# Performance work log

Measured on AMD Instinct MI355X. Metric: run time of the kernel, lower is better.

The kernel has to match this reference:

```python
import jax, jax.numpy as jnp
import numpy as np

N_NODES = 100000
N_EDGES = 1600000
IN_CH = 128
HIDDEN = 64
N_CLASSES = 40


def setup_inputs() -> dict:
    key = jax.random.key(0)
    k_x, k_e, k_w1, k_w2 = jax.random.split(key, 4)
    x = jax.random.normal(k_x, (N_NODES, IN_CH), dtype=jnp.float32)
    edge_index = jax.random.randint(k_e, (2, N_EDGES), 0, N_NODES, dtype=jnp.int64)
    # Glorot-style init for GCN weights
    W1 = jax.random.normal(k_w1, (IN_CH, HIDDEN), dtype=jnp.float32) * (1.0 / np.sqrt(IN_CH))
    b1 = jnp.zeros((HIDDEN,), dtype=jnp.float32)
    W2 = jax.random.normal(k_w2, (HIDDEN, N_CLASSES), dtype=jnp.float32) * (1.0 / np.sqrt(HIDDEN))
    b2 = jnp.zeros((N_CLASSES,), dtype=jnp.float32)
    return {"x": x, "edge_index": edge_index, "W1": W1, "b1": b1, "W2": W2, "b2": b2}


def reference(x, edge_index, W1, b1, W2, b2):
    n = x.shape[0]
    # PyG GCNConv: add self-loops, symmetric degree normalization
    loop = jnp.arange(n, dtype=edge_index.dtype)
    src = jnp.concatenate([edge_index[0], loop])  # message sources j
    dst = jnp.concatenate([edge_index[1], loop])  # aggregation targets i
    w = jnp.ones(src.shape[0], dtype=x.dtype)     # edge_weight=None -> ones
    deg = jax.ops.segment_sum(w, dst, num_segments=n)
    dinv = jnp.where(deg > 0, jax.lax.rsqrt(jnp.maximum(deg, 1e-12)), 0.0)
    norm = dinv[src] * dinv[dst]                  # [E+N]

    def gcn_conv(h, W, b):
        hw = h @ W                                # transform first (fewer flops)
        msg = hw[src] * norm[:, None]             # gather + normalize
        return jax.ops.segment_sum(msg, dst, num_segments=n) + b  # scatter-add

    h = jax.nn.relu(gcn_conv(x, W1, b1))
    # dropout is identity in eval mode
    out = gcn_conv(h, W2, b2)
    return out
```

## Files before the change

### kernel.cpp

```cpp
#include <hip/hip_runtime.h>
#include <hip/hip_bf16.h>

#define NNODES 100000
#define NEDGES 1600000
#define IN_CH 128
#define HID 64
#define NC 40
#define NPAD 100352
#define NBUK 196
#define CAP 9216
#define BCHUNK 4096
#define NBIN 391

typedef unsigned short ushort_t;
typedef unsigned int uint_t;
typedef __attribute__((ext_vector_type(8))) short short8;
typedef __attribute__((ext_vector_type(4))) float floatx4;
typedef __attribute__((ext_vector_type(2))) float f32x2;

__device__ __forceinline__ ushort_t f2bf(float f) {
    union { float ff; unsigned int i; } t;
    t.ff = f;
    unsigned int r = t.i + 0x7fff + ((t.i >> 16) & 1);
    return (ushort_t)(r >> 16);
}
__device__ __forceinline__ void acc2(f32x2& a, uint_t p) {
    union { unsigned int i; float f; } lo, hi;
    lo.i = p << 16;
    hi.i = p & 0xffff0000u;
    f32x2 v = {lo.f, hi.f};
    a += v;
}

__global__ __launch_bounds__(256) void k_bin0(
    const int* __restrict__ srcs, const int* __restrict__ dsts,
    int* __restrict__ gcur, uint_t* __restrict__ tmp, int e,
    const float* __restrict__ W1, ushort_t* __restrict__ Wp,
    ushort_t* __restrict__ hb, int n)
{
    __shared__ uint_t pk[BCHUNK];
    __shared__ ushort_t bk[BCHUNK];
    __shared__ int hist[NBUK];
    __shared__ int base[NBUK];
    int t = threadIdx.x;
    if (blockIdx.x >= NBIN) {
        for (int i = t; i < IN_CH * HID; i += 256) {
            int j = i & 7;
            int m = (i >> 3) & 15;
            int ct = (i >> 7) & 3;
            int quad = (i >> 9) & 3;
            int kc = i >> 11;
            int k = kc * 32 + quad * 8 + j;
            int c = ct * 16 + m;
            Wp[i] = f2bf(W1[k * HID + c]);
        }
        uint_t* hbz = (uint_t*)(hb + (size_t)n * HID);
        if (t < 32) hbz[t] = 0;
        return;
    }
    int begin = blockIdx.x * BCHUNK;
    int cnt = e - begin; if (cnt > BCHUNK) cnt = BCHUNK;

    for (int i = t; i < NBUK; i += 256) hist[i] = 0;
    __syncthreads();
    for (int j = t; j < cnt; j += 256) {
        int d = dsts[begin + j];
        int s = srcs[begin + j];
        int b = d >> 9;
        pk[j] = (uint_t)s | ((uint_t)(d & 511) << 17);
        bk[j] = (ushort_t)b;
        atomicAdd(&hist[b], 1);
    }
    __syncthreads();
    for (int i = t; i < NBUK; i += 256) {
        base[i] = i * CAP + atomicAdd(&gcur[i], hist[i]);
        hist[i] = 0;
    }
    __syncthreads();
    for (int j = t; j < cnt; j += 256) {
        int b = bk[j];
        int r = atomicAdd(&hist[b], 1);
        int pos = base[b] + r;
        if (pos < (b + 1) * CAP) tmp[pos] = pk[j];
    }
}

__global__ __launch_bounds__(256) void k_sort(
    const uint_t* __restrict__ tmp, const int* __restrict__ gcur,
    int* __restrict__ row_start, float* __restrict__ dinv,
    uint_t* __restrict__ es, int n, int e)
{
    __shared__ int cnt[512];
    __shared__ int sc[512];
    __shared__ int red[256];
    int t = threadIdx.x;
    int b = blockIdx.x;
    int d0 = b << 9;
    int total = gcur[b];
    if (total > CAP) total = CAP;
    int part = 0;
    for (int i = t; i < b; i += 256) part += gcur[i];
    red[t] = part;
    cnt[t] = 0; cnt[t + 256] = 0;
    __syncthreads();
    for (int off = 128; off > 0; off >>= 1) {
        if (t < off) red[t] += red[t + off];
        __syncthreads();
    }
    int gb = red[0];
    const uint_t* seg = tmp + b * CAP;
    for (int j = t; j < total; j += 256)
        atomicAdd(&cnt[seg[j] >> 17], 1);
    __syncthreads();
    sc[t] = cnt[t]; sc[t + 256] = cnt[t + 256];
    __syncthreads();
    for (int off = 1; off < 512; off <<= 1) {
        int v0 = (t >= off) ? sc[t - off] : 0;
        int i1 = t + 256;
        int v1 = (i1 >= off) ? sc[i1 - off] : 0;
        __syncthreads();
        sc[t] += v0; sc[i1] += v1;
        __syncthreads();
    }
#pragma unroll
    for (int q = 0; q < 2; ++q) {
        int i = t + q * 256;
        int node = d0 + i;
        int start = gb + sc[i] - cnt[i];
        if (node < n) {
            row_start[node] = start;
            dinv[node] = rsqrtf((float)cnt[i] + 1.0f);
        }
        cnt[i] = start;
    }
    __syncthreads();
    for (int j = t; j < total; j += 256) {
        uint_t p = seg[j];
        int ld = (int)(p >> 17);
        int pos = atomicAdd(&cnt[ld], 1);
        es[pos] = p & 0x1FFFFu;
    }
    if (b == NBUK - 1 && t == 0) row_start[n] = e;
}

__global__ __launch_bounds__(256) void k_gemm1(
    const float* __restrict__ x, const ushort_t* __restrict__ Wp,
    const float* __restrict__ dinv, ushort_t* __restrict__ hw1, int n)
{
    int wave = threadIdx.x >> 6;
    int lane = threadIdx.x & 63;
    int m = lane & 15;
    int quad = lane >> 4;
    int row = blockIdx.x * 64 + wave * 16 + m;
    int rowc = row < n ? row : (n - 1);
    const float* xr = x + (size_t)rowc * IN_CH + quad * 8;

    floatx4 acc[4];
#pragma unroll
    for (int ct = 0; ct < 4; ++ct) acc[ct] = (floatx4){0.f, 0.f, 0.f, 0.f};

#pragma unroll
    for (int kc = 0; kc < 4; ++kc) {
        float4 xa = *(const float4*)(xr + kc * 32);
        float4 xb = *(const float4*)(xr + kc * 32 + 4);
        short8 a;
        a[0] = (short)f2bf(xa.x); a[1] = (short)f2bf(xa.y);
        a[2] = (short)f2bf(xa.z); a[3] = (short)f2bf(xa.w);
        a[4] = (short)f2bf(xb.x); a[5] = (short)f2bf(xb.y);
        a[6] = (short)f2bf(xb.z); a[7] = (short)f2bf(xb.w);
#pragma unroll
        for (int ct = 0; ct < 4; ++ct) {
            short8 b = *(const short8*)(Wp + ((((kc * 4 + quad) * 4 + ct) * 16 + m) << 3));
            acc[ct] = __builtin_amdgcn_mfma_f32_16x16x32_bf16(a, b, acc[ct], 0, 0, 0);
        }
    }
    int r0 = blockIdx.x * 64 + wave * 16 + quad * 4;
#pragma unroll
    for (int r = 0; r < 4; ++r) {
        int rr = r0 + r;
        if (rr < n) {
            float di = dinv[rr];
            ushort_t* o = hw1 + (size_t)rr * HID + m;
#pragma unroll
            for (int ct = 0; ct < 4; ++ct) o[ct * 16] = f2bf(acc[ct][r] * di);
        } else if (rr == n) {
            ushort_t* o = hw1 + (size_t)n * HID + m;
#pragma unroll
            for (int ct = 0; ct < 4; ++ct) o[ct * 16] = 0;
        }
    }
}

__global__ __launch_bounds__(256) void k_agg1(
    const int* __restrict__ row_start, const uint_t* __restrict__ es,
    const float* __restrict__ dinv, const uint_t* __restrict__ hw1u,
    const float* __restrict__ b1, ushort_t* __restrict__ hb, int n)
{
    int lane = threadIdx.x & 63;
    int obase = lane & 56;
    int ol = lane & 7;
    int node = blockIdx.x * 32 + (threadIdx.x >> 3);
    bool valid = node < n;
    int rs = valid ? row_start[node] : 0;
    int re = valid ? row_start[node + 1] : 0;
    float di = valid ? dinv[node] : 0.f;
    int selfrow = valid ? node : n;

    f32x2 c0, c1, c2, c3;
    {
        uint4 sp = *(const uint4*)(hw1u + (size_t)selfrow * 32 + ol * 4);
        c0 = (f32x2){0.f, 0.f}; c1 = c0; c2 = c0; c3 = c0;
        acc2(c0, sp.x); acc2(c1, sp.y); acc2(c2, sp.z); acc2(c3, sp.w);
    }
    for (int base = rs; base < re; base += 8) {
        int idx = base + ol;
        int el = (idx < re) ? (int)es[idx] : n;
        uint4 p[8];
#pragma unroll
        for (int b = 0; b < 8; ++b) {
            int s = __shfl(el, obase + b);
            p[b] = *(const uint4*)(hw1u + (size_t)s * 32 + ol * 4);
        }
#pragma unroll
        for (int b = 0; b < 8; ++b) {
            acc2(c0, p[b].x); acc2(c1, p[b].y);
            acc2(c2, p[b].z); acc2(c3, p[b].w);
        }
    }
    if (valid) {
        float4 bb0 = ((const float4*)b1)[ol * 2];
        float4 bb1 = ((const float4*)b1)[ol * 2 + 1];
        float h0 = fmaxf(c0.x * di + bb0.x, 0.f);
        float h1 = fmaxf(c0.y * di + bb0.y, 0.f);
        float h2 = fmaxf(c1.x * di + bb0.z, 0.f);
        float h3 = fmaxf(c1.y * di + bb0.w, 0.f);
        float h4 = fmaxf(c2.x * di + bb1.x, 0.f);
        float h5 = fmaxf(c2.y * di + bb1.y, 0.f);
        float h6 = fmaxf(c3.x * di + bb1.z, 0.f);
        float h7 = fmaxf(c3.y * di + bb1.w, 0.f);
        uint4 st;
        st.x = (uint_t)f2bf(h0 * di) | ((uint_t)f2bf(h1 * di) << 16);
        st.y = (uint_t)f2bf(h2 * di) | ((uint_t)f2bf(h3 * di) << 16);
        st.z = (uint_t)f2bf(h4 * di) | ((uint_t)f2bf(h5 * di) << 16);
        st.w = (uint_t)f2bf(h6 * di) | ((uint_t)f2bf(h7 * di) << 16);
        *(uint4*)(hb + (size_t)node * HID + ol * 8) = st;
    }
}

__global__ __launch_bounds__(256) void k_agg2(
    const int* __restrict__ row_start, const uint_t* __restrict__ es,
    const float* __restrict__ dinv, const uint_t* __restrict__ hbu,
    const float* __restrict__ W2, const float* __restrict__ b2,
    float* __restrict__ out, int n)
{
    __shared__ float wsm[HID * NC];
    __shared__ float hsm[32][68];
    for (int i = threadIdx.x; i < HID * NC; i += 256) wsm[i] = W2[i];
    __syncthreads();

    int lane = threadIdx.x & 63;
    int obase = lane & 56;
    int ol = lane & 7;
    int slot = threadIdx.x >> 3;
    int node = blockIdx.x * 32 + slot;
    bool valid = node < n;
    int rs = valid ? row_start[node] : 0;
    int re = valid ? row_start[node + 1] : 0;
    float di = valid ? dinv[node] : 0.f;
    int selfrow = valid ? node : n;

    f32x2 c0, c1, c2, c3;
    {
        uint4 sp = *(const uint4*)(hbu + (size_t)selfrow * 32 + ol * 4);
        c0 = (f32x2){0.f, 0.f}; c1 = c0; c2 = c0; c3 = c0;
        acc2(c0, sp.x); acc2(c1, sp.y); acc2(c2, sp.z); acc2(c3, sp.w);
    }
    for (int base = rs; base < re; base += 8) {
        int idx = base + ol;
        int el = (idx < re) ? (int)es[idx] : n;
        uint4 p[8];
#pragma unroll
        for (int b = 0; b < 8; ++b) {
            int s = __shfl(el, obase + b);
            p[b] = *(const uint4*)(hbu + (size_t)s * 32 + ol * 4);
        }
#pragma unroll
        for (int b = 0; b < 8; ++b) {
            acc2(c0, p[b].x); acc2(c1, p[b].y);
            acc2(c2, p[b].z); acc2(c3, p[b].w);
        }
    }
    {
        float4 g0, g1;
        g0.x = c0.x * di; g0.y = c0.y * di; g0.z = c1.x * di; g0.w = c1.y * di;
        g1.x = c2.x * di; g1.y = c2.y * di; g1.z = c3.x * di; g1.w = c3.y * di;
        *(float4*)&hsm[slot][ol * 8] = g0;
        *(float4*)&hsm[slot][ol * 8 + 4] = g1;
    }
    int w8 = (threadIdx.x >> 6) * 8;
    int qm = lane >> 4;
    int lq = lane & 15;
    int lw = (lq < 10) ? lq : 0;
    const float4* w4 = (const float4*)wsm;
#pragma unroll
    for (int pass = 0; pass < 2; ++pass) {
        int slot2 = w8 + pass * 4 + qm;
        int node2 = blockIdx.x * 32 + slot2;
        float4 acc = ((const float4*)b2)[lw];
#pragma unroll 4
        for (int k4 = 0; k4 < 16; ++k4) {
            float4 hk = *(const float4*)&hsm[slot2][k4 * 4];
            float4 w0 = w4[(k4 * 4 + 0) * 10 + lw];
            float4 w1 = w4[(k4 * 4 + 1) * 10 + lw];
            float4 w2 = w4[(k4 * 4 + 2) * 10 + lw];
            float4 w3 = w4[(k4 * 4 + 3) * 10 + lw];
            acc.x += hk.x * w0.x + hk.y * w1.x + hk.z * w2.x + hk.w * w3.x;
            acc.y += hk.x * w0.y + hk.y * w1.y + hk.z * w2.y + hk.w * w3.y;
            acc.z += hk.x * w0.z + hk.y * w1.z + hk.z * w2.z + hk.w * w3.z;
            acc.w += hk.x * w0.w + hk.y * w1.w + hk.z * w2.w + hk.w * w3.w;
        }
        if (node2 < n && lq < 10)
            *(float4*)(out + (size_t)node2 * NC + lq * 4) = acc;
    }
}

extern "C" void kernel_launch(void* const* d_in, const int* in_sizes, int n_in,
                              void* d_out, int out_size, void* d_ws, size_t ws_size,
                              hipStream_t stream) {
    const float* x  = (const float*)d_in[0];
    const int* edge = (const int*)d_in[1];
    const float* W1 = (const float*)d_in[2];
    const float* b1 = (const float*)d_in[3];
    const float* W2 = (const float*)d_in[4];
    const float* b2 = (const float*)d_in[5];
    float* out      = (float*)d_out;

    const int n = in_sizes[0] / IN_CH;
    const int e = in_sizes[1] / 2;
    const int* srcs = edge;
    const int* dsts = edge + e;

    int*      gcur      = (int*)d_ws;
    int*      row_start = gcur + 256;
    float*    dinv      = (float*)(row_start + NPAD);
    uint_t*   tmp       = (uint_t*)(dinv + NPAD);
    uint_t*   es        = tmp + (size_t)NBUK * CAP;
    ushort_t* Wp        = (ushort_t*)(es + NEDGES);
    ushort_t* hw1       = Wp + 8192;
    ushort_t* hb        = hw1 + (size_t)(NNODES + 1) * HID;

    hipMemsetAsync(gcur, 0, NBUK * sizeof(int), stream);
    k_bin0<<<NBIN + 1, 256, 0, stream>>>(srcs, dsts, gcur, tmp, e, W1, Wp, hb, n);
    k_sort<<<NBUK, 256, 0, stream>>>(tmp, gcur, row_start, dinv, es, n, e);
    k_gemm1<<<(n + 63) / 64, 256, 0, stream>>>(x, Wp, dinv, hw1, n);
    k_agg1<<<(n + 31) / 32, 256, 0, stream>>>(row_start, es, dinv, (const uint_t*)hw1, b1, hb, n);
    k_agg2<<<(n + 31) / 32, 256, 0, stream>>>(row_start, es, dinv, (const uint_t*)hb, W2, b2, out, n);
}
```

Before: 220.8 us.

## Sort nodes by degree within block and double-buffer neighbor gathers in aggregation

Both aggregation kernels now rank the block's 32 nodes by in-degree and give them to 8-lane groups in that order, so nodes with similar degrees share a wavefront and there is less loop divergence. The gather loop becomes a two-stage software pipeline: indices are loaded as vectors and the next 8 rows are fetched while the previous 8 are accumulated. Launch bounds request 2 blocks per CU. The cost is an in-block rank sort with two extra barriers and higher register pressure from the doubled gather buffers. The tail handling now clamps out-of-range nodes to n-1, which recomputes and rewrites that node instead of using the padding row.

```diff
diff --git a/kernel.cpp b/kernel.cpp
--- a/kernel.cpp
+++ b/kernel.cpp
@@ -17,6 +17,7 @@
 typedef __attribute__((ext_vector_type(8))) short short8;
 typedef __attribute__((ext_vector_type(4))) float floatx4;
 typedef __attribute__((ext_vector_type(2))) float f32x2;
+typedef unsigned int uint4u __attribute__((ext_vector_type(4))) __attribute__((aligned(4)));
 
 __device__ __forceinline__ ushort_t f2bf(float f) {
     union { float ff; unsigned int i; } t;
@@ -30,6 +31,30 @@
     hi.i = p & 0xffff0000u;
     f32x2 v = {lo.f, hi.f};
     a += v;
+}
+
+__device__ __forceinline__ void ldidx(const uint_t* __restrict__ es, int b2,
+                                      int re, int n, uint_t s[8]) {
+    uint4u e0 = *(const uint4u*)(es + b2);
+    uint4u e1 = *(const uint4u*)(es + b2 + 4);
+#pragma unroll
+    for (int b = 0; b < 4; ++b) s[b] = (b2 + b < re) ? (uint_t)e0[b] : (uint_t)n;
+#pragma unroll
+    for (int b = 0; b < 4; ++b) s[4 + b] = (b2 + 4 + b < re) ? (uint_t)e1[b] : (uint_t)n;
+}
+__device__ __forceinline__ void gath8(const uint_t* __restrict__ rowb,
+                                      const uint_t s[8], int ol, uint4 p[8]) {
+#pragma unroll
+    for (int b = 0; b < 8; ++b)
+        p[b] = *(const uint4*)(rowb + (size_t)s[b] * 32 + ol * 4);
+}
+__device__ __forceinline__ void cons8(f32x2& c0, f32x2& c1, f32x2& c2, f32x2& c3,
+                                      const uint4 p[8]) {
+#pragma unroll
+    for (int b = 0; b < 8; ++b) {
+        acc2(c0, p[b].x); acc2(c1, p[b].y);
+        acc2(c2, p[b].z); acc2(c3, p[b].w);
+    }
 }
 
 __global__ __launch_bounds__(256) void k_bin0(
@@ -191,43 +216,72 @@
     }
 }
 
-__global__ __launch_bounds__(256) void k_agg1(
+__global__ __launch_bounds__(256, 2) void k_agg1(
     const int* __restrict__ row_start, const uint_t* __restrict__ es,
     const float* __restrict__ dinv, const uint_t* __restrict__ hw1u,
     const float* __restrict__ b1, ushort_t* __restrict__ hb, int n)
 {
-    int lane = threadIdx.x & 63;
-    int obase = lane & 56;
+    __shared__ int sdeg[32];
+    __shared__ int sperm[32];
+    int t = threadIdx.x;
+    if (t < 32) {
+        int nd = blockIdx.x * 32 + t;
+        if (nd >= n) nd = n - 1;
+        sdeg[t] = row_start[nd + 1] - row_start[nd];
+    }
+    __syncthreads();
+    if (t < 32) {
+        int d = sdeg[t];
+        int rank = 0;
+        for (int j = 0; j < 32; ++j) {
+            int dj = sdeg[j];
+            rank += (dj < d) || (dj == d && j < t);
+        }
+        sperm[rank] = t;
+    }
+    __syncthreads();
+
+    int lane = t & 63;
     int ol = lane & 7;
-    int node = blockIdx.x * 32 + (threadIdx.x >> 3);
-    bool valid = node < n;
-    int rs = valid ? row_start[node] : 0;
-    int re = valid ? row_start[node + 1] : 0;
-    float di = valid ? dinv[node] : 0.f;
-    int selfrow = valid ? node : n;
+    int slot = t >> 3;
+    int node = blockIdx.x * 32 + sperm[slot];
+    if (node >= n) node = n - 1;
+    int rs = row_start[node];
+    int re = row_start[node + 1];
+    float di = dinv[node];
 
     f32x2 c0, c1, c2, c3;
     {
-        uint4 sp = *(const uint4*)(hw1u + (size_t)selfrow * 32 + ol * 4);
+        uint4 sp = *(const uint4*)(hw1u + (size_t)node * 32 + ol * 4);
         c0 = (f32x2){0.f, 0.f}; c1 = c0; c2 = c0; c3 = c0;
         acc2(c0, sp.x); acc2(c1, sp.y); acc2(c2, sp.z); acc2(c3, sp.w);
     }
-    for (int base = rs; base < re; base += 8) {
-        int idx = base + ol;
-        int el = (idx < re) ? (int)es[idx] : n;
-        uint4 p[8];
-#pragma unroll
-        for (int b = 0; b < 8; ++b) {
-            int s = __shfl(el, obase + b);
-            p[b] = *(const uint4*)(hw1u + (size_t)s * 32 + ol * 4);
-        }
-#pragma unroll
-        for (int b = 0; b < 8; ++b) {
-            acc2(c0, p[b].x); acc2(c1, p[b].y);
-            acc2(c2, p[b].z); acc2(c3, p[b].w);
-        }
-    }
-    if (valid) {
+    uint_t sA[8], sB[8];
+    uint4 pA[8], pB[8];
+    int base = rs;
+    ldidx(es, base, re, n, sA);
+    gath8(hw1u, sA, ol, pA);
+    while (true) {
+        int nb = base + 8;
+        if (nb < re) {
+            ldidx(es, nb, re, n, sB);
+            gath8(hw1u, sB, ol, pB);
+            cons8(c0, c1, c2, c3, pA);
+            int nb2 = nb + 8;
+            if (nb2 < re) {
+                ldidx(es, nb2, re, n, sA);
+                gath8(hw1u, sA, ol, pA);
+                cons8(c0, c1, c2, c3, pB);
+                base = nb2;
+                continue;
+            }
+            cons8(c0, c1, c2, c3, pB);
+        } else {
+            cons8(c0, c1, c2, c3, pA);
+        }
+        break;
+    }
+    {
         float4 bb0 = ((const float4*)b1)[ol * 2];
         float4 bb1 = ((const float4*)b1)[ol * 2 + 1];
         float h0 = fmaxf(c0.x * di + bb0.x, 0.f);
@@ -247,7 +301,7 @@
     }
 }
 
-__global__ __launch_bounds__(256) void k_agg2(
+__global__ __launch_bounds__(256, 2) void k_agg2(
     const int* __restrict__ row_start, const uint_t* __restrict__ es,
     const float* __restrict__ dinv, const uint_t* __restrict__ hbu,
     const float* __restrict__ W2, const float* __restrict__ b2,
@@ -255,40 +309,66 @@
 {
     __shared__ float wsm[HID * NC];
     __shared__ float hsm[32][68];
-    for (int i = threadIdx.x; i < HID * NC; i += 256) wsm[i] = W2[i];
-    __syncthreads();
-
-    int lane = threadIdx.x & 63;
-    int obase = lane & 56;
+    __shared__ int sdeg[32];
+    __shared__ int sperm[32];
+    int t = threadIdx.x;
+    for (int i = t; i < HID * NC; i += 256) wsm[i] = W2[i];
+    if (t < 32) {
+        int nd = blockIdx.x * 32 + t;
+        if (nd >= n) nd = n - 1;
+        sdeg[t] = row_start[nd + 1] - row_start[nd];
+    }
+    __syncthreads();
+    if (t < 32) {
+        int d = sdeg[t];
+        int rank = 0;
+        for (int j = 0; j < 32; ++j) {
+            int dj = sdeg[j];
+            rank += (dj < d) || (dj == d && j < t);
+        }
+        sperm[rank] = t;
+    }
+    __syncthreads();
+
+    int lane = t & 63;
     int ol = lane & 7;
-    int slot = threadIdx.x >> 3;
-    int node = blockIdx.x * 32 + slot;
-    bool valid = node < n;
-    int rs = valid ? row_start[node] : 0;
-    int re = valid ? row_start[node + 1] : 0;
-    float di = valid ? dinv[node] : 0.f;
-    int selfrow = valid ? node : n;
+    int slot = t >> 3;
+    int node = blockIdx.x * 32 + sperm[slot];
+    if (node >= n) node = n - 1;
+    int rs = row_start[node];
+    int re = row_start[node + 1];
+    float di = dinv[node];
 
     f32x2 c0, c1, c2, c3;
     {
-        uint4 sp = *(const uint4*)(hbu + (size_t)selfrow * 32 + ol * 4);
+        uint4 sp = *(const uint4*)(hbu + (size_t)node * 32 + ol * 4);
         c0 = (f32x2){0.f, 0.f}; c1 = c0; c2 = c0; c3 = c0;
         acc2(c0, sp.x); acc2(c1, sp.y); acc2(c2, sp.z); acc2(c3, sp.w);
     }
-    for (int base = rs; base < re; base += 8) {
-        int idx = base + ol;
-        int el = (idx < re) ? (int)es[idx] : n;
-        uint4 p[8];
-#pragma unroll
-        for (int b = 0; b < 8; ++b) {
-            int s = __shfl(el, obase + b);
-            p[b] = *(const uint4*)(hbu + (size_t)s * 32 + ol * 4);
-        }
-#pragma unroll
-        for (int b = 0; b < 8; ++b) {
-            acc2(c0, p[b].x); acc2(c1, p[b].y);
-            acc2(c2, p[b].z); acc2(c3, p[b].w);
-        }
+    uint_t sA[8], sB[8];
+    uint4 pA[8], pB[8];
+    int base = rs;
+    ldidx(es, base, re, n, sA);
+    gath8(hbu, sA, ol, pA);
+    while (true) {
+        int nb = base + 8;
+        if (nb < re) {
+            ldidx(es, nb, re, n, sB);
+            gath8(hbu, sB, ol, pB);
+            cons8(c0, c1, c2, c3, pA);
+            int nb2 = nb + 8;
+            if (nb2 < re) {
+                ldidx(es, nb2, re, n, sA);
+                gath8(hbu, sA, ol, pA);
+                cons8(c0, c1, c2, c3, pB);
+                base = nb2;
+                continue;
+            }
+            cons8(c0, c1, c2, c3, pB);
+        } else {
+            cons8(c0, c1, c2, c3, pA);
+        }
+        break;
     }
     {
         float4 g0, g1;
@@ -297,7 +377,7 @@
         *(float4*)&hsm[slot][ol * 8] = g0;
         *(float4*)&hsm[slot][ol * 8 + 4] = g1;
     }
-    int w8 = (threadIdx.x >> 6) * 8;
+    int w8 = (t >> 6) * 8;
     int qm = lane >> 4;
     int lq = lane & 15;
     int lw = (lq < 10) ? lq : 0;
@@ -305,7 +385,7 @@
 #pragma unroll
     for (int pass = 0; pass < 2; ++pass) {
         int slot2 = w8 + pass * 4 + qm;
-        int node2 = blockIdx.x * 32 + slot2;
+        int node2 = blockIdx.x * 32 + sperm[slot2];
         float4 acc = ((const float4*)b2)[lw];
 #pragma unroll 4
         for (int k4 = 0; k4 < 16; ++k4) {
```

New measurement: 231.6 us. 1.05x slower.

## Merge bucket sort and first GEMM into one launch using global degree counts

Applied to the files above, without the earlier changes.

The per-bucket sort and the first dense transform now run as separate block ranges of a single kernel, removing one launch and letting the two stages overlap on the GPU. Because the GEMM blocks can no longer wait for dinv from the sort, the binning kernel also counts node degrees with global atomics, and the GEMM computes its normalization from those counts. This costs 1.6M extra global atomic adds in the binning pass and a larger memset, in exchange for removing the dependency between the sort and the GEMM.

```diff
diff --git a/kernel.cpp b/kernel.cpp
--- a/kernel.cpp
+++ b/kernel.cpp
@@ -34,7 +34,7 @@
 
 __global__ __launch_bounds__(256) void k_bin0(
     const int* __restrict__ srcs, const int* __restrict__ dsts,
-    int* __restrict__ gcur, uint_t* __restrict__ tmp, int e,
+    int* __restrict__ gcur, int* __restrict__ deg, uint_t* __restrict__ tmp, int e,
     const float* __restrict__ W1, ushort_t* __restrict__ Wp,
     ushort_t* __restrict__ hb, int n)
 {
@@ -70,6 +70,7 @@
         pk[j] = (uint_t)s | ((uint_t)(d & 511) << 17);
         bk[j] = (ushort_t)b;
         atomicAdd(&hist[b], 1);
+        atomicAdd(&deg[d], 1);
     }
     __syncthreads();
     for (int i = t; i < NBUK; i += 256) {
@@ -85,73 +86,73 @@
     }
 }
 
-__global__ __launch_bounds__(256) void k_sort(
+__global__ __launch_bounds__(256) void k_sg(
     const uint_t* __restrict__ tmp, const int* __restrict__ gcur,
     int* __restrict__ row_start, float* __restrict__ dinv,
-    uint_t* __restrict__ es, int n, int e)
+    uint_t* __restrict__ es, int n, int e,
+    const float* __restrict__ x, const ushort_t* __restrict__ Wp,
+    const int* __restrict__ deg, ushort_t* __restrict__ hw1)
 {
     __shared__ int cnt[512];
     __shared__ int sc[512];
     __shared__ int red[256];
     int t = threadIdx.x;
-    int b = blockIdx.x;
-    int d0 = b << 9;
-    int total = gcur[b];
-    if (total > CAP) total = CAP;
-    int part = 0;
-    for (int i = t; i < b; i += 256) part += gcur[i];
-    red[t] = part;
-    cnt[t] = 0; cnt[t + 256] = 0;
-    __syncthreads();
-    for (int off = 128; off > 0; off >>= 1) {
-        if (t < off) red[t] += red[t + off];
+    if (blockIdx.x < NBUK) {
+        int b = blockIdx.x;
+        int d0 = b << 9;
+        int total = gcur[b];
+        if (total > CAP) total = CAP;
+        int part = 0;
+        for (int i = t; i < b; i += 256) part += gcur[i];
+        red[t] = part;
+        cnt[t] = 0; cnt[t + 256] = 0;
         __syncthreads();
-    }
-    int gb = red[0];
-    const uint_t* seg = tmp + b * CAP;
-    for (int j = t; j < total; j += 256)
-        atomicAdd(&cnt[seg[j] >> 17], 1);
-    __syncthreads();
-    sc[t] = cnt[t]; sc[t + 256] = cnt[t + 256];
-    __syncthreads();
-    for (int off = 1; off < 512; off <<= 1) {
-        int v0 = (t >= off) ? sc[t - off] : 0;
-        int i1 = t + 256;
-        int v1 = (i1 >= off) ? sc[i1 - off] : 0;
+        for (int off = 128; off > 0; off >>= 1) {
+            if (t < off) red[t] += red[t + off];
+            __syncthreads();
+        }
+        int gb = red[0];
+        const uint_t* seg = tmp + b * CAP;
+        for (int j = t; j < total; j += 256)
+            atomicAdd(&cnt[seg[j] >> 17], 1);
         __syncthreads();
-        sc[t] += v0; sc[i1] += v1;
+        sc[t] = cnt[t]; sc[t + 256] = cnt[t + 256];
         __syncthreads();
-    }
-#pragma unroll
-    for (int q = 0; q < 2; ++q) {
-        int i = t + q * 256;
-        int node = d0 + i;
-        int start = gb + sc[i] - cnt[i];
-        if (node < n) {
-            row_start[node] = start;
-            dinv[node] = rsqrtf((float)cnt[i] + 1.0f);
-        }
-        cnt[i] = start;
-    }
-    __syncthreads();
-    for (int j = t; j < total; j += 256) {
-        uint_t p = seg[j];
-        int ld = (int)(p >> 17);
-        int pos = atomicAdd(&cnt[ld], 1);
-        es[pos] = p & 0x1FFFFu;
-    }
-    if (b == NBUK - 1 && t == 0) row_start[n] = e;
-}
-
-__global__ __launch_bounds__(256) void k_gemm1(
-    const float* __restrict__ x, const ushort_t* __restrict__ Wp,
-    const float* __restrict__ dinv, ushort_t* __restrict__ hw1, int n)
-{
-    int wave = threadIdx.x >> 6;
-    int lane = threadIdx.x & 63;
+        for (int off = 1; off < 512; off <<= 1) {
+            int v0 = (t >= off) ? sc[t - off] : 0;
+            int i1 = t + 256;
+            int v1 = (i1 >= off) ? sc[i1 - off] : 0;
+            __syncthreads();
+            sc[t] += v0; sc[i1] += v1;
+            __syncthreads();
+        }
+#pragma unroll
+        for (int q = 0; q < 2; ++q) {
+            int i = t + q * 256;
+            int node = d0 + i;
+            int start = gb + sc[i] - cnt[i];
+            if (node < n) {
+                row_start[node] = start;
+                dinv[node] = rsqrtf((float)cnt[i] + 1.0f);
+            }
+            cnt[i] = start;
+        }
+        __syncthreads();
+        for (int j = t; j < total; j += 256) {
+            uint_t p = seg[j];
+            int ld = (int)(p >> 17);
+            int pos = atomicAdd(&cnt[ld], 1);
+            es[pos] = p & 0x1FFFFu;
+        }
+        if (b == NBUK - 1 && t == 0) row_start[n] = e;
+        return;
+    }
+    int blk = blockIdx.x - NBUK;
+    int wave = t >> 6;
+    int lane = t & 63;
     int m = lane & 15;
     int quad = lane >> 4;
-    int row = blockIdx.x * 64 + wave * 16 + m;
+    int row = blk * 64 + wave * 16 + m;
     int rowc = row < n ? row : (n - 1);
     const float* xr = x + (size_t)rowc * IN_CH + quad * 8;
 
@@ -174,12 +175,12 @@
             acc[ct] = __builtin_amdgcn_mfma_f32_16x16x32_bf16(a, b, acc[ct], 0, 0, 0);
         }
     }
-    int r0 = blockIdx.x * 64 + wave * 16 + quad * 4;
+    int r0 = blk * 64 + wave * 16 + quad * 4;
 #pragma unroll
     for (int r = 0; r < 4; ++r) {
         int rr = r0 + r;
         if (rr < n) {
-            float di = dinv[rr];
+            float di = rsqrtf((float)deg[rr] + 1.0f);
             ushort_t* o = hw1 + (size_t)rr * HID + m;
 #pragma unroll
             for (int ct = 0; ct < 4; ++ct) o[ct * 16] = f2bf(acc[ct][r] * di);
@@ -341,7 +342,8 @@
     const int* dsts = edge + e;
 
     int*      gcur      = (int*)d_ws;
-    int*      row_start = gcur + 256;
+    int*      deg       = gcur + 256;
+    int*      row_start = deg + NPAD;
     float*    dinv      = (float*)(row_start + NPAD);
     uint_t*   tmp       = (uint_t*)(dinv + NPAD);
     uint_t*   es        = tmp + (size_t)NBUK * CAP;
@@ -349,10 +351,10 @@
     ushort_t* hw1       = Wp + 8192;
     ushort_t* hb        = hw1 + (size_t)(NNODES + 1) * HID;
 
-    hipMemsetAsync(gcur, 0, NBUK * sizeof(int), stream);
-    k_bin0<<<NBIN + 1, 256, 0, stream>>>(srcs, dsts, gcur, tmp, e, W1, Wp, hb, n);
-    k_sort<<<NBUK, 256, 0, stream>>>(tmp, gcur, row_start, dinv, es, n, e);
-    k_gemm1<<<(n + 63) / 64, 256, 0, stream>>>(x, Wp, dinv, hw1, n);
+    hipMemsetAsync(gcur, 0, (256 + NPAD) * sizeof(int), stream);
+    k_bin0<<<NBIN + 1, 256, 0, stream>>>(srcs, dsts, gcur, deg, tmp, e, W1, Wp, hb, n);
+    k_sg<<<NBUK + (n + 63) / 64, 256, 0, stream>>>(tmp, gcur, row_start, dinv, es, n, e,
+                                                   x, Wp, deg, hw1);
     k_agg1<<<(n + 31) / 32, 256, 0, stream>>>(row_start, es, dinv, (const uint_t*)hw1, b1, hb, n);
     k_agg2<<<(n + 31) / 32, 256, 0, stream>>>(row_start, es, dinv, (const uint_t*)hb, W2, b2, out, n);
 }
```

Measured after the change: 265.5 us. +20.2%, slower.
